# Kernel optimization log

Measured on AMD Instinct MI355X. Metric: run time of the kernel, lower is better.

## Reference

```python
import jax, jax.numpy as jnp
import numpy as np

B, N, DIM = 1, 4096, 1024
HEADS, DIM_HEAD = 12, 8
POST_LOG_SCALE = 1.0
SCALE = DIM_HEAD ** -0.5


def setup_inputs() -> dict:
    key = jax.random.key(0)
    kx, kw = jax.random.split(key)
    x = jax.random.normal(kx, (B, N, DIM), dtype=jnp.float32)
    # torch nn.Linear(dim, heads*dim_head*2, bias=False) weight: [2*heads*dim_head, dim]
    W = jax.random.normal(kw, (2 * HEADS * DIM_HEAD, DIM), dtype=jnp.float32) * (DIM ** -0.5)
    return {"x": x, "W": W}


def reference(x, W):
    b, n, _ = x.shape
    # linear: x @ W^T -> [b, n, 2*h*d]; rearrange '(qk h d) -> qk b h n d'
    proj = jnp.einsum('bnc,oc->bno', x, W)
    proj = proj.reshape(b, n, 2, HEADS, DIM_HEAD)
    q = jnp.transpose(proj[:, :, 0], (0, 2, 1, 3))  # [b, h, n, d]
    k = jnp.transpose(proj[:, :, 1], (0, 2, 1, 3))  # [b, h, n, d]
    # small-d QK matmul -> [b, h, n, n]
    gates = jnp.einsum('bhid,bhjd->bhij', q, k) * SCALE
    gates = jax.nn.log_sigmoid(gates) * POST_LOG_SCALE
    # causal_mask = triu(ones, diagonal=0); masked_fill -> zero on/above diagonal
    i = jnp.arange(n)[:, None]
    j = jnp.arange(n)[None, :]
    keep = j < i  # strictly lower-triangular entries survive
    gates = jnp.where(keep, gates, 0.0)
    # flip-cumsum-flip == reverse cumulative sum along last axis
    gates = jax.lax.cumsum(gates, axis=3, reverse=True)
    return gates
```

## Files before the change

### kernel.cpp

```cpp
#include <hip/hip_runtime.h>

#define NTOK 4096
#define DIMC 1024
#define HEADS 12
#define DH 8
#define QSCALE 0.35355339059327373f
#define LOG2E  1.4426950408889634f
#define LN2    0.6931471805599453f

#define KOFF (HEADS * NTOK * DH)

__global__ __launch_bounds__(256) void k1_proj(const float* __restrict__ x,
                                               const float* __restrict__ W,
                                               float* __restrict__ qk) {
    __shared__ float xs[8 * 1028];
    const int t = threadIdx.x;
    const int row0 = blockIdx.x * 8;

    const float4* x4 = (const float4*)(x + (size_t)row0 * DIMC);
    #pragma unroll
    for (int i = 0; i < 8; ++i) {
        int f = t + i * 256;
        int r = f >> 8;
        int c4 = f & 255;
        float4 v = x4[f];
        *(float4*)(&xs[r * 1028 + c4 * 4]) = v;
    }
    __syncthreads();

    const int g  = t >> 2;
    const int rg = t & 3;

    float acc[2][3];
    #pragma unroll
    for (int a = 0; a < 2; ++a)
        #pragma unroll
        for (int m = 0; m < 3; ++m) acc[a][m] = 0.f;

    const float* w0 = W + (size_t)(3 * g) * DIMC;
    #pragma unroll 2
    for (int c = 0; c < DIMC; c += 4) {
        float4 w[3];
        #pragma unroll
        for (int m = 0; m < 3; ++m)
            w[m] = *(const float4*)(w0 + (size_t)m * DIMC + c);
        #pragma unroll
        for (int a = 0; a < 2; ++a) {
            float4 xv = *(const float4*)(&xs[(rg * 2 + a) * 1028 + c]);
            #pragma unroll
            for (int m = 0; m < 3; ++m) {
                acc[a][m] = fmaf(xv.x, w[m].x,
                            fmaf(xv.y, w[m].y,
                            fmaf(xv.z, w[m].z,
                            fmaf(xv.w, w[m].w, acc[a][m]))));
            }
        }
    }

    #pragma unroll
    for (int m = 0; m < 3; ++m) {
        int o   = 3 * g + m;
        int qkf = (o >= 96) ? 1 : 0;
        int oo  = o - 96 * qkf;
        int h   = oo >> 3;
        int d   = oo & 7;
        #pragma unroll
        for (int a = 0; a < 2; ++a) {
            int n = row0 + rg * 2 + a;
            float v = acc[a][m];
            if (!qkf) {
                qk[((size_t)h * NTOK + n) * DH + d] = v * QSCALE;
            } else {
                qk[KOFF + ((size_t)h * DH + d) * NTOK + n] = v;
            }
        }
    }
}

__device__ __forceinline__ float log_sigmoid(float s) {
    float mn = fminf(s, 0.f);
    float z  = __builtin_amdgcn_exp2f(fabsf(s) * -LOG2E);
    return mn - LN2 * __builtin_amdgcn_logf(1.f + z);
}

__global__ __launch_bounds__(256) void k2_gates(const float* __restrict__ qk,
                                                float* __restrict__ out) {
    const int bid  = blockIdx.x;
    const int h    = bid >> 9;
    const int i0   = (bid & 511) << 3;
    const int t    = threadIdx.x;
    const int lane = t & 63;
    const int wid  = t >> 6;

    __shared__ __align__(16) float qs[64];
    __shared__ float wtot[2][4][8];

    if (t < 64) {
        int r = t >> 3, d = t & 7;
        qs[t] = qk[((size_t)h * NTOK + i0 + r) * DH + d];
    }
    __syncthreads();

    const float* ks = qk + KOFF + (size_t)h * DH * NTOK;
    float* obase = out + ((size_t)h * NTOK + i0) * NTOK;

    float carry[8];
    #pragma unroll
    for (int r = 0; r < 8; ++r) carry[r] = 0.f;

    #pragma unroll
    for (int cc = 0; cc < 4; ++cc) {
        const int c  = 3 - cc;
        const int j0 = c * 1024 + 4 * t;
        float* op = obase + j0;

        if (1024 * c >= i0 + 7) {
            float4 z; z.x = 0.f; z.y = 0.f; z.z = 0.f; z.w = 0.f;
            #pragma unroll
            for (int r = 0; r < 8; ++r)
                *(float4*)(op + (size_t)r * NTOK) = z;
        } else {
            float4 kv[8];
            #pragma unroll
            for (int d = 0; d < 8; ++d)
                kv[d] = *(const float4*)(ks + (size_t)d * NTOK + j0);

            float ov[8][4], tot[8], tsave[8];
            #pragma unroll
            for (int r = 0; r < 8; ++r) {
                const int ir = i0 + r;
                float4 qa = *(const float4*)(&qs[r * 8]);
                float4 qb = *(const float4*)(&qs[r * 8 + 4]);
                float s0 = 0.f, s1 = 0.f, s2 = 0.f, s3 = 0.f;
                #pragma unroll
                for (int d = 0; d < 8; ++d) {
                    float qd = (d == 0) ? qa.x : (d == 1) ? qa.y : (d == 2) ? qa.z : (d == 3) ? qa.w
                             : (d == 4) ? qb.x : (d == 5) ? qb.y : (d == 6) ? qb.z : qb.w;
                    s0 = fmaf(qd, kv[d].x, s0);
                    s1 = fmaf(qd, kv[d].y, s1);
                    s2 = fmaf(qd, kv[d].z, s2);
                    s3 = fmaf(qd, kv[d].w, s3);
                }
                float g0 = (j0 + 0 < ir) ? log_sigmoid(s0) : 0.f;
                float g1 = (j0 + 1 < ir) ? log_sigmoid(s1) : 0.f;
                float g2 = (j0 + 2 < ir) ? log_sigmoid(s2) : 0.f;
                float g3 = (j0 + 3 < ir) ? log_sigmoid(s3) : 0.f;
                g2 += g3; g1 += g2; g0 += g1;
                ov[r][0] = g0; ov[r][1] = g1; ov[r][2] = g2; ov[r][3] = g3;
                tot[r] = g0; tsave[r] = g0;
            }

            #pragma unroll
            for (int off = 1; off < 64; off <<= 1) {
                #pragma unroll
                for (int r = 0; r < 8; ++r) {
                    float v = __shfl_down(tot[r], off, 64);
                    if (lane + off < 64) tot[r] += v;
                }
            }

            if (lane == 0) {
                #pragma unroll
                for (int r = 0; r < 8; ++r) wtot[cc & 1][wid][r] = tot[r];
            }
            __syncthreads();

            #pragma unroll
            for (int r = 0; r < 8; ++r) {
                float w0 = wtot[cc & 1][0][r];
                float w1 = wtot[cc & 1][1][r];
                float w2 = wtot[cc & 1][2][r];
                float w3 = wtot[cc & 1][3][r];
                float later = (wid == 0) ? (w1 + w2 + w3)
                            : (wid == 1) ? (w2 + w3)
                            : (wid == 2) ? w3 : 0.f;
                float base = (tot[r] - tsave[r]) + later + carry[r];
                carry[r] += w0 + w1 + w2 + w3;
                float4 v;
                v.x = ov[r][0] + base;
                v.y = ov[r][1] + base;
                v.z = ov[r][2] + base;
                v.w = ov[r][3] + base;
                *(float4*)(op + (size_t)r * NTOK) = v;
            }
        }
    }
}

extern "C" void kernel_launch(void* const* d_in, const int* in_sizes, int n_in,
                              void* d_out, int out_size, void* d_ws, size_t ws_size,
                              hipStream_t stream) {
    const float* x = (const float*)d_in[0];
    const float* W = (const float*)d_in[1];
    float* out = (float*)d_out;
    float* qk  = (float*)d_ws;

    hipLaunchKernelGGL(k1_proj, dim3(NTOK / 8), dim3(256), 0, stream, x, W, qk);
    hipLaunchKernelGGL(k2_gates, dim3(HEADS * NTOK / 8), dim3(256), 0, stream, qk, out);
}
```

Baseline: 216.6 us.

## Give each wave two rows and scan per wave to skip upper-triangle compute

The gates kernel now assigns two output rows to each 64-lane wave. Each wave walks 256-column chunks from right to left and does the reverse scan with wave shuffles and a register carry, so the shared-memory cross-wave reduction and __syncthreads go away. Chunks fully above the diagonal are written as zeros without computing them, at a finer granularity than the earlier 1024-column test. Output stores become nontemporal. Per-wave work is now imbalanced across rows, and K is reloaded by every wave rather than shared across the block.

```diff
diff --git a/kernel.cpp b/kernel.cpp
--- a/kernel.cpp
+++ b/kernel.cpp
@@ -8,6 +8,8 @@
 #define LOG2E  1.4426950408889634f
 #define LN2    0.6931471805599453f
 
+typedef float f4 __attribute__((ext_vector_type(4)));
+
 #define KOFF (HEADS * NTOK * DH)
 
 __global__ __launch_bounds__(256) void k1_proj(const float* __restrict__ x,
@@ -17,14 +19,14 @@
     const int t = threadIdx.x;
     const int row0 = blockIdx.x * 8;
 
-    const float4* x4 = (const float4*)(x + (size_t)row0 * DIMC);
+    const f4* x4 = (const f4*)(x + (size_t)row0 * DIMC);
     #pragma unroll
     for (int i = 0; i < 8; ++i) {
         int f = t + i * 256;
         int r = f >> 8;
         int c4 = f & 255;
-        float4 v = x4[f];
-        *(float4*)(&xs[r * 1028 + c4 * 4]) = v;
+        f4 v = x4[f];
+        *(f4*)(&xs[r * 1028 + c4 * 4]) = v;
     }
     __syncthreads();
 
@@ -40,13 +42,13 @@
     const float* w0 = W + (size_t)(3 * g) * DIMC;
     #pragma unroll 2
     for (int c = 0; c < DIMC; c += 4) {
-        float4 w[3];
+        f4 w[3];
         #pragma unroll
         for (int m = 0; m < 3; ++m)
-            w[m] = *(const float4*)(w0 + (size_t)m * DIMC + c);
+            w[m] = *(const f4*)(w0 + (size_t)m * DIMC + c);
         #pragma unroll
         for (int a = 0; a < 2; ++a) {
-            float4 xv = *(const float4*)(&xs[(rg * 2 + a) * 1028 + c]);
+            f4 xv = *(const f4*)(&xs[(rg * 2 + a) * 1028 + c]);
             #pragma unroll
             for (int m = 0; m < 3; ++m) {
                 acc[a][m] = fmaf(xv.x, w[m].x,
@@ -91,99 +93,83 @@
     const int t    = threadIdx.x;
     const int lane = t & 63;
     const int wid  = t >> 6;
+    const int r0   = i0 + 2 * wid;
 
-    __shared__ __align__(16) float qs[64];
-    __shared__ float wtot[2][4][8];
-
-    if (t < 64) {
-        int r = t >> 3, d = t & 7;
-        qs[t] = qk[((size_t)h * NTOK + i0 + r) * DH + d];
-    }
-    __syncthreads();
+    const float* qrow = qk + ((size_t)h * NTOK + r0) * DH;
+    float qa[8], qb[8];
+    #pragma unroll
+    for (int d = 0; d < 8; ++d) { qa[d] = qrow[d]; qb[d] = qrow[DH + d]; }
 
     const float* ks = qk + KOFF + (size_t)h * DH * NTOK;
-    float* obase = out + ((size_t)h * NTOK + i0) * NTOK;
+    float* o0 = out + ((size_t)h * NTOK + r0) * NTOK;
+    float* o1 = o0 + NTOK;
 
-    float carry[8];
-    #pragma unroll
-    for (int r = 0; r < 8; ++r) carry[r] = 0.f;
+    const int ccmax = r0 >> 8;
 
-    #pragma unroll
-    for (int cc = 0; cc < 4; ++cc) {
-        const int c  = 3 - cc;
-        const int j0 = c * 1024 + 4 * t;
-        float* op = obase + j0;
+    f4 z = (f4)(0.f);
+    for (int cc = 15; cc > ccmax; --cc) {
+        const int j0 = cc * 256 + 4 * lane;
+        __builtin_nontemporal_store(z, (f4*)(o0 + j0));
+        __builtin_nontemporal_store(z, (f4*)(o1 + j0));
+    }
 
-        if (1024 * c >= i0 + 7) {
-            float4 z; z.x = 0.f; z.y = 0.f; z.z = 0.f; z.w = 0.f;
-            #pragma unroll
-            for (int r = 0; r < 8; ++r)
-                *(float4*)(op + (size_t)r * NTOK) = z;
-        } else {
-            float4 kv[8];
-            #pragma unroll
-            for (int d = 0; d < 8; ++d)
-                kv[d] = *(const float4*)(ks + (size_t)d * NTOK + j0);
+    float carry0 = 0.f, carry1 = 0.f;
+    for (int cc = ccmax; cc >= 0; --cc) {
+        const int j0 = cc * 256 + 4 * lane;
 
-            float ov[8][4], tot[8], tsave[8];
-            #pragma unroll
-            for (int r = 0; r < 8; ++r) {
-                const int ir = i0 + r;
-                float4 qa = *(const float4*)(&qs[r * 8]);
-                float4 qb = *(const float4*)(&qs[r * 8 + 4]);
-                float s0 = 0.f, s1 = 0.f, s2 = 0.f, s3 = 0.f;
-                #pragma unroll
-                for (int d = 0; d < 8; ++d) {
-                    float qd = (d == 0) ? qa.x : (d == 1) ? qa.y : (d == 2) ? qa.z : (d == 3) ? qa.w
-                             : (d == 4) ? qb.x : (d == 5) ? qb.y : (d == 6) ? qb.z : qb.w;
-                    s0 = fmaf(qd, kv[d].x, s0);
-                    s1 = fmaf(qd, kv[d].y, s1);
-                    s2 = fmaf(qd, kv[d].z, s2);
-                    s3 = fmaf(qd, kv[d].w, s3);
-                }
-                float g0 = (j0 + 0 < ir) ? log_sigmoid(s0) : 0.f;
-                float g1 = (j0 + 1 < ir) ? log_sigmoid(s1) : 0.f;
-                float g2 = (j0 + 2 < ir) ? log_sigmoid(s2) : 0.f;
-                float g3 = (j0 + 3 < ir) ? log_sigmoid(s3) : 0.f;
-                g2 += g3; g1 += g2; g0 += g1;
-                ov[r][0] = g0; ov[r][1] = g1; ov[r][2] = g2; ov[r][3] = g3;
-                tot[r] = g0; tsave[r] = g0;
-            }
+        f4 kv[8];
+        #pragma unroll
+        for (int d = 0; d < 8; ++d)
+            kv[d] = *(const f4*)(ks + (size_t)d * NTOK + j0);
 
-            #pragma unroll
-            for (int off = 1; off < 64; off <<= 1) {
-                #pragma unroll
-                for (int r = 0; r < 8; ++r) {
-                    float v = __shfl_down(tot[r], off, 64);
-                    if (lane + off < 64) tot[r] += v;
-                }
-            }
+        float a0 = 0.f, a1 = 0.f, a2 = 0.f, a3 = 0.f;
+        float b0 = 0.f, b1 = 0.f, b2 = 0.f, b3 = 0.f;
+        #pragma unroll
+        for (int d = 0; d < 8; ++d) {
+            a0 = fmaf(qa[d], kv[d].x, a0);
+            a1 = fmaf(qa[d], kv[d].y, a1);
+            a2 = fmaf(qa[d], kv[d].z, a2);
+            a3 = fmaf(qa[d], kv[d].w, a3);
+            b0 = fmaf(qb[d], kv[d].x, b0);
+            b1 = fmaf(qb[d], kv[d].y, b1);
+            b2 = fmaf(qb[d], kv[d].z, b2);
+            b3 = fmaf(qb[d], kv[d].w, b3);
+        }
 
-            if (lane == 0) {
-                #pragma unroll
-                for (int r = 0; r < 8; ++r) wtot[cc & 1][wid][r] = tot[r];
-            }
-            __syncthreads();
+        float g0[4], g1[4];
+        g0[0] = (j0 + 0 < r0) ? log_sigmoid(a0) : 0.f;
+        g0[1] = (j0 + 1 < r0) ? log_sigmoid(a1) : 0.f;
+        g0[2] = (j0 + 2 < r0) ? log_sigmoid(a2) : 0.f;
+        g0[3] = (j0 + 3 < r0) ? log_sigmoid(a3) : 0.f;
+        const int r1 = r0 + 1;
+        g1[0] = (j0 + 0 < r1) ? log_sigmoid(b0) : 0.f;
+        g1[1] = (j0 + 1 < r1) ? log_sigmoid(b1) : 0.f;
+        g1[2] = (j0 + 2 < r1) ? log_sigmoid(b2) : 0.f;
+        g1[3] = (j0 + 3 < r1) ? log_sigmoid(b3) : 0.f;
 
-            #pragma unroll
-            for (int r = 0; r < 8; ++r) {
-                float w0 = wtot[cc & 1][0][r];
-                float w1 = wtot[cc & 1][1][r];
-                float w2 = wtot[cc & 1][2][r];
-                float w3 = wtot[cc & 1][3][r];
-                float later = (wid == 0) ? (w1 + w2 + w3)
-                            : (wid == 1) ? (w2 + w3)
-                            : (wid == 2) ? w3 : 0.f;
-                float base = (tot[r] - tsave[r]) + later + carry[r];
-                carry[r] += w0 + w1 + w2 + w3;
-                float4 v;
-                v.x = ov[r][0] + base;
-                v.y = ov[r][1] + base;
-                v.z = ov[r][2] + base;
-                v.w = ov[r][3] + base;
-                *(float4*)(op + (size_t)r * NTOK) = v;
-            }
+        g0[2] += g0[3]; g0[1] += g0[2]; g0[0] += g0[1];
+        g1[2] += g1[3]; g1[1] += g1[2]; g1[0] += g1[1];
+        const float t0 = g0[0], t1 = g1[0];
+
+        float s0 = t0, s1 = t1;
+        #pragma unroll
+        for (int off = 1; off < 64; off <<= 1) {
+            float v0 = __shfl_down(s0, off, 64);
+            float v1 = __shfl_down(s1, off, 64);
+            if (lane + off < 64) { s0 += v0; s1 += v1; }
         }
+        const float base0 = (s0 - t0) + carry0;
+        const float base1 = (s1 - t1) + carry1;
+        carry0 += __shfl(s0, 0, 64);
+        carry1 += __shfl(s1, 0, 64);
+
+        f4 v0, v1;
+        v0.x = g0[0] + base0; v0.y = g0[1] + base0;
+        v0.z = g0[2] + base0; v0.w = g0[3] + base0;
+        v1.x = g1[0] + base1; v1.y = g1[1] + base1;
+        v1.z = g1[2] + base1; v1.w = g1[3] + base1;
+        __builtin_nontemporal_store(v0, (f4*)(o0 + j0));
+        __builtin_nontemporal_store(v1, (f4*)(o1 + j0));
     }
 }
 
```

Measured after the change: 209.3 us. -3.4%, faster.
